# Kernel tuning notes

Measured on AMD Instinct MI355X. Metric: run time of the kernel, lower is better.

## Reference

```python
import jax, jax.numpy as jnp
import numpy as np

N = 100000      # num nodes
F_IN = 512      # dataset.num_features
HID = 32        # hardcoded hidden dim in CRD
C = 40          # dataset.num_classes
E = 3200000     # num edges


def setup_inputs() -> dict:
    key = jax.random.key(0)
    ks = jax.random.split(key, 16)
    def glorot(k, shape):
        lim = float(np.sqrt(6.0 / (shape[0] + shape[1])))
        return jax.random.uniform(k, shape, jnp.float32, -lim, lim)
    inp = {
        "x": jax.random.normal(ks[0], (N, F_IN), dtype=jnp.float32),
        "edge_index": jax.random.randint(ks[1], (2, E), 0, N, dtype=jnp.int32),
        # CRD 1: two GCNConv(F_IN -> HID)
        "W1a": glorot(ks[2], (F_IN, HID)), "b1a": jnp.zeros((HID,), jnp.float32),
        "W1b": glorot(ks[3], (F_IN, HID)), "b1b": jnp.zeros((HID,), jnp.float32),
        # CRD 2: two GCNConv(F_IN -> HID)
        "W2a": glorot(ks[4], (F_IN, HID)), "b2a": jnp.zeros((HID,), jnp.float32),
        "W2b": glorot(ks[5], (F_IN, HID)), "b2b": jnp.zeros((HID,), jnp.float32),
        # CLS: two GCNConv(HID -> C)
        "W3a": glorot(ks[6], (HID, C)), "b3a": jnp.zeros((C,), jnp.float32),
        "W3b": glorot(ks[7], (HID, C)), "b3b": jnp.zeros((C,), jnp.float32),
    }
    return inp


def reference(x, edge_index, W1a, b1a, W1b, b1b, W2a, b2a, W2b, b2b, W3a, b3a, W3b, b3b):
    n = x.shape[0]
    # GCN normalization with self-loops (PyG gcn_norm, cached=True -> shared)
    loop = jnp.arange(n, dtype=edge_index.dtype)
    src = jnp.concatenate([edge_index[0], loop])  # [E+N]
    dst = jnp.concatenate([edge_index[1], loop])
    deg = jax.ops.segment_sum(jnp.ones_like(dst, jnp.float32), dst, num_segments=n)
    dinv = jnp.where(deg > 0, jax.lax.rsqrt(jnp.maximum(deg, 1e-12)), 0.0)
    norm = dinv[src] * dinv[dst]  # [E+N]

    def gcn(h, W, b):
        hw = h @ W                                     # [n, d_out] project first
        msg = hw[src] * norm[:, None]                  # gather + scale
        return jax.ops.segment_sum(msg, dst, num_segments=n) + b  # scatter-add

    # CRD 1 (dropout is identity in eval)
    x1 = jax.nn.relu(gcn(x, W1a, b1a)) + jax.nn.relu(gcn(x, W1b, b1b))
    # CRD 2
    x2 = jax.nn.relu(gcn(x, W2a, b2a)) + jax.nn.relu(gcn(x, W2b, b2b))
    # CLS
    xs = x1 + x2
    out = jax.nn.log_softmax(gcn(xs, W3a, b3a) + gcn(xs, W3b, b3b), axis=1)
    return out
```

## Files before the change

### kernel.cpp

```cpp
#include <hip/hip_runtime.h>
#include <hip/hip_bf16.h>
#include <math.h>

typedef __attribute__((ext_vector_type(8))) short short8;
typedef __attribute__((ext_vector_type(4))) float f32x4;

__device__ inline ushort f2bf(float f) {
    uint u = __builtin_bit_cast(uint, f);
    u += 0x7fffu + ((u >> 16) & 1u);
    return (ushort)(u >> 16);
}
__device__ inline float bf2f(ushort h) {
    return __builtin_bit_cast(float, (uint)h << 16);
}


#define NB   256
#define BKE  2048
#define CAP  16384
#define MAXBE 16384

__device__ inline int bucket_of(int d, int W, float recipW) {
    int g = (int)((float)d * recipW);
    if (g > NB - 1) g = NB - 1;
    while (d < g * W) --g;
    while (d >= (g + 1) * W) ++g;
    return g;
}

__global__ void initcur_kernel(int* __restrict__ cursor256) {
    cursor256[threadIdx.x] = threadIdx.x * CAP;
}

__global__ __launch_bounds__(256) void bucket_kernel(const int* __restrict__ src, const int* __restrict__ dst,
                                                     int* __restrict__ cursor256, int* __restrict__ epk,
                                                     int E, int W, float recipW) {
    __shared__ int hist[NB];
    __shared__ int base[NB];
    int tid = threadIdx.x;
    int e0 = blockIdx.x * BKE;
    int e1 = e0 + BKE; if (e1 > E) e1 = E;
    if (e0 >= E) return;
    hist[tid] = 0;
    __syncthreads();
    int myp[8], myg[8], myr[8];
    #pragma unroll
    for (int it = 0; it < 8; ++it) {
        int e = e0 + tid + it * 256;
        myg[it] = -1;
        if (e < e1) {
            int d = dst[e];
            int g = bucket_of(d, W, recipW);
            myp[it] = src[e] | ((d - g * W) << 17);
            myg[it] = g;
            myr[it] = atomicAdd(&hist[g], 1);
        }
    }
    __syncthreads();
    base[tid] = atomicAdd(&cursor256[tid], hist[tid]);
    __syncthreads();
    #pragma unroll
    for (int it = 0; it < 8; ++it)
        if (myg[it] >= 0)
            epk[base[myg[it]] + myr[it]] = myp[it];
}

__global__ void scanpost_kernel(const int* __restrict__ cursor256, int* __restrict__ bbase) {
    __shared__ int tot[NB];
    int b = threadIdx.x;
    int cnt = cursor256[b] - b * CAP;
    tot[b] = cnt;
    __syncthreads();
    for (int off = 1; off < NB; off <<= 1) {
        int t = (b >= off) ? tot[b - off] : 0;
        __syncthreads();
        tot[b] += t;
        __syncthreads();
    }
    bbase[b] = tot[b] - cnt;
    if (b == NB - 1) bbase[NB] = tot[NB - 1];
}

__global__ __launch_bounds__(256) void sortcsr_kernel(const int* __restrict__ epk,
                                                      const int* __restrict__ bbase,
                                                      int* __restrict__ csr, int* __restrict__ offs,
                                                      float* __restrict__ dinv, int N, int W, int E) {
    __shared__ int lcnt[512];
    __shared__ int lofs[513];
    __shared__ int tmp[256];
    __shared__ int lcsr[MAXBE];
    int b = blockIdx.x;
    int lo = b * W;
    int nloc = N - lo; if (nloc > W) nloc = W; if (nloc < 0) nloc = 0;
    int gbase = bbase[b];
    int cnt = bbase[b + 1] - gbase;
    int ebk = b * CAP;
    int tid = threadIdx.x;
    lcnt[2 * tid] = 0; lcnt[2 * tid + 1] = 0;
    __syncthreads();
    for (int e = tid; e < cnt; e += 256)
        atomicAdd(&lcnt[epk[ebk + e] >> 17], 1);
    __syncthreads();
    int a0 = lcnt[2 * tid], a1 = lcnt[2 * tid + 1];
    int psum = a0 + a1;
    tmp[tid] = psum;
    __syncthreads();
    for (int off = 1; off < 256; off <<= 1) {
        int t = (tid >= off) ? tmp[tid - off] : 0;
        __syncthreads();
        tmp[tid] += t;
        __syncthreads();
    }
    int excl = tmp[tid] - psum;
    lofs[2 * tid] = excl;
    lofs[2 * tid + 1] = excl + a0;
    lcnt[2 * tid] = excl;
    lcnt[2 * tid + 1] = excl + a0;
    if (tid == 255) lofs[512] = tmp[255];
    __syncthreads();
    for (int t = tid; t < nloc; t += 256) {
        offs[lo + t] = gbase + lofs[t];
        int deg = lofs[t + 1] - lofs[t];
        dinv[lo + t] = rsqrtf((float)(deg + 1));
    }
    if (b == NB - 1 && tid == 0) offs[N] = E;
    for (int e = tid; e < cnt; e += 256) {
        int p = epk[ebk + e];
        int pos = atomicAdd(&lcnt[p >> 17], 1);
        int sv = p & 0x1FFFF;
        if (pos < MAXBE) lcsr[pos] = sv;
        else csr[gbase + pos] = sv;
    }
    __syncthreads();
    int ne = cnt; if (ne > MAXBE) ne = MAXBE;
    for (int e = tid; e < ne; e += 256) csr[gbase + e] = lcsr[e];
}


__global__ __launch_bounds__(256) void prep_kernel(const float* __restrict__ W1a, const float* __restrict__ W1b,
                                                   const float* __restrict__ W2a, const float* __restrict__ W2b,
                                                   const float* __restrict__ b1a, const float* __restrict__ b1b,
                                                   const float* __restrict__ b2a, const float* __restrict__ b2b,
                                                   const float* __restrict__ W3a, const float* __restrict__ W3b,
                                                   const float* __restrict__ b3a, const float* __restrict__ b3b,
                                                   ushort* __restrict__ Wt, float* __restrict__ bcat,
                                                   float* __restrict__ W3s, float* __restrict__ b3s) {
    int idx = blockIdx.x * 256 + threadIdx.x;
    if (idx < 128 * 512) {
        int row = idx >> 9, kk = idx & 511;
        int cstore = (kk >> 3) & 7;
        int clog = cstore ^ (row & 7);
        int klog = (kk & ~63) | (clog << 3) | (kk & 7);
        const float* Wsrc = (row < 32) ? W1a : (row < 64) ? W1b : (row < 96) ? W2a : W2b;
        Wt[idx] = f2bf(Wsrc[klog * 32 + (row & 31)]);
    }
    if (idx < 1280) W3s[idx] = W3a[idx] + W3b[idx];
    if (idx < 128) {
        const float* b = (idx < 32) ? b1a : (idx < 64) ? b1b : (idx < 96) ? b2a : b2b;
        bcat[idx] = b[idx & 31];
    }
    if (idx < 40) b3s[idx] = b3a[idx] + b3b[idx];
}


#define GBM 64

__global__ __launch_bounds__(256) void gemm_mfma(const float* __restrict__ X,
                                                 const ushort* __restrict__ Wt,
                                                 const float* __restrict__ dinv,
                                                 ushort* __restrict__ HWp, int N) {
    __shared__ float  Af[64 * 64];
    __shared__ ushort Bl[128 * 64];
    const int tid = threadIdx.x;
    const int lane = tid & 63;
    const int wave = tid >> 6;
    const int rQ = lane & 15, g = lane >> 4;
    const int rowBase = blockIdx.x * GBM;

    const float* agsrc[4];
    #pragma unroll
    for (int i = 0; i < 4; ++i) {
        int q = (i * 4 + wave) * 64 + lane;
        int row = q >> 4, c = q & 15;
        int rowg = rowBase + row; if (rowg > N - 1) rowg = N - 1;
        agsrc[i] = X + (size_t)rowg * 512 + ((c ^ (row & 15)) << 2);
    }
    const ushort* bgsrc[4];
    #pragma unroll
    for (int i = 0; i < 4; ++i) {
        int q = (i * 4 + wave) * 64 + lane;
        int row = q >> 3, c = q & 7;
        bgsrc[i] = Wt + (size_t)row * 512 + (c << 3);
    }

    f32x4 acc[4][2] = {};

#define STAGE(s)                                                              \
    {                                                                         \
        _Pragma("unroll")                                                     \
        for (int i = 0; i < 4; ++i)                                           \
            __builtin_amdgcn_global_load_lds(                                 \
                (const uint*)(agsrc[i] + (s) * 64),                           \
                (uint*)&Af[(i * 4 + wave) * 256], 16, 0, 0);                  \
        _Pragma("unroll")                                                     \
        for (int i = 0; i < 4; ++i)                                           \
            __builtin_amdgcn_global_load_lds(                                 \
                (const uint*)(bgsrc[i] + (s) * 64),                           \
                (uint*)&Bl[(i * 4 + wave) * 512], 16, 0, 0);                  \
    }

#define COMPUTE()                                                             \
    {                                                                         \
        short8 bfr[2][2];                                                     \
        _Pragma("unroll")                                                     \
        for (int ct2 = 0; ct2 < 2; ++ct2) {                                   \
            int brow = wave * 32 + ct2 * 16 + rQ;                             \
            _Pragma("unroll")                                                 \
            for (int sub = 0; sub < 2; ++sub)                                 \
                bfr[ct2][sub] = *(const short8*)(&Bl[brow * 64 + (((sub * 4 + g) ^ (brow & 7)) << 3)]); \
        }                                                                     \
        _Pragma("unroll")                                                     \
        for (int rt = 0; rt < 4; ++rt) {                                      \
            int arw = rt * 16 + rQ;                                           \
            _Pragma("unroll")                                                 \
            for (int sub = 0; sub < 2; ++sub) {                               \
                int c0 = (sub * 4 + g) * 2;                                   \
                float4 lo = *(const float4*)(&Af[arw * 64 + ((c0 ^ (arw & 15)) << 2)]);       \
                float4 hi = *(const float4*)(&Af[arw * 64 + (((c0 + 1) ^ (arw & 15)) << 2)]); \
                union { short8 s8; __hip_bfloat162 h[4]; } u;                 \
                u.h[0] = __float22bfloat162_rn({lo.x, lo.y});                 \
                u.h[1] = __float22bfloat162_rn({lo.z, lo.w});                 \
                u.h[2] = __float22bfloat162_rn({hi.x, hi.y});                 \
                u.h[3] = __float22bfloat162_rn({hi.z, hi.w});                 \
                _Pragma("unroll")                                             \
                for (int ct2 = 0; ct2 < 2; ++ct2)                             \
                    acc[rt][ct2] = __builtin_amdgcn_mfma_f32_16x16x32_bf16(   \
                        u.s8, bfr[ct2][sub], acc[rt][ct2], 0, 0, 0);          \
            }                                                                 \
        }                                                                     \
    }

    for (int s = 0; s < 8; ++s) {
        STAGE(s);
        __syncthreads();
        COMPUTE();
        __syncthreads();
    }

    #pragma unroll
    for (int rt = 0; rt < 4; ++rt) {
        #pragma unroll
        for (int j = 0; j < 4; ++j) {
            int r = rowBase + rt * 16 + g * 4 + j;
            if (r < N) {
                float dv = dinv[r];
                #pragma unroll
                for (int ct2 = 0; ct2 < 2; ++ct2) {
                    int c = wave * 32 + ct2 * 16 + rQ;
                    HWp[(size_t)r * 128 + c] = f2bf(acc[rt][ct2][j] * dv);
                }
            }
        }
    }
#undef STAGE
#undef COMPUTE
}


__global__ __launch_bounds__(256) void agg128(const ushort* __restrict__ HWp, const float* __restrict__ dinv,
                                              const int* __restrict__ offs, const int* __restrict__ csr,
                                              const float* __restrict__ bcat, ushort* __restrict__ xsp, int N) {
    int t = blockIdx.x * 256 + threadIdx.x;
    int node = t >> 4, c = t & 15;
    if (node >= N) return;
    const short8* H = (const short8*)HWp;
    short8 h = H[(size_t)node * 16 + c];
    float a[8];
    #pragma unroll
    for (int i = 0; i < 8; ++i) a[i] = bf2f((ushort)h[i]);
    int j = offs[node];
    int e1 = offs[node + 1];
    int jend = j + ((e1 - j) & ~7);
    for (; j < jend; j += 8) {
        int s[8];
        #pragma unroll
        for (int q = 0; q < 8; ++q) s[q] = csr[j + q];
        short8 v[8];
        #pragma unroll
        for (int q = 0; q < 8; ++q) v[q] = H[(size_t)s[q] * 16 + c];
        #pragma unroll
        for (int q = 0; q < 8; ++q)
            #pragma unroll
            for (int i = 0; i < 8; ++i) a[i] += bf2f((ushort)v[q][i]);
    }
    for (; j < e1; ++j) {
        short8 v = H[(size_t)csr[j] * 16 + c];
        #pragma unroll
        for (int i = 0; i < 8; ++i) a[i] += bf2f((ushort)v[i]);
    }
    float di = dinv[node];
    float4 b0 = *(const float4*)(bcat + c * 8);
    float4 b1 = *(const float4*)(bcat + c * 8 + 4);
    float bb[8] = {b0.x, b0.y, b0.z, b0.w, b1.x, b1.y, b1.z, b1.w};
    float r[8];
    #pragma unroll
    for (int i = 0; i < 8; ++i) r[i] = fmaxf(di * a[i] + bb[i], 0.f);
    #pragma unroll
    for (int i = 0; i < 8; ++i) { r[i] += __shfl_xor(r[i], 4); r[i] += __shfl_xor(r[i], 8); }
    if ((c & 12) == 0) {
        union { short8 s8; ushort us[8]; } o;
        #pragma unroll
        for (int i = 0; i < 8; ++i) o.us[i] = f2bf(r[i] * di);
        *(short8*)(xsp + (size_t)node * 32 + c * 8) = o.s8;
    }
}


__global__ __launch_bounds__(256) void agg32(const ushort* __restrict__ xsp, const float* __restrict__ dinv,
                                             const int* __restrict__ offs, const int* __restrict__ csr,
                                             float* __restrict__ axs, int N) {
    int t = blockIdx.x * 256 + threadIdx.x;
    int node = t >> 2, l = t & 3;
    if (node >= N) return;
    const short8* Xr = (const short8*)xsp;
    short8 h = Xr[(size_t)node * 4 + l];
    float a[8];
    #pragma unroll
    for (int i = 0; i < 8; ++i) a[i] = bf2f((ushort)h[i]);
    int j = offs[node];
    int e1 = offs[node + 1];
    int jend = j + ((e1 - j) & ~7);
    for (; j < jend; j += 8) {
        int s[8];
        #pragma unroll
        for (int q = 0; q < 8; ++q) s[q] = csr[j + q];
        short8 v[8];
        #pragma unroll
        for (int q = 0; q < 8; ++q) v[q] = Xr[(size_t)s[q] * 4 + l];
        #pragma unroll
        for (int q = 0; q < 8; ++q)
            #pragma unroll
            for (int i = 0; i < 8; ++i) a[i] += bf2f((ushort)v[q][i]);
    }
    for (; j < e1; ++j) {
        short8 v = Xr[(size_t)csr[j] * 4 + l];
        #pragma unroll
        for (int i = 0; i < 8; ++i) a[i] += bf2f((ushort)v[i]);
    }
    float di = dinv[node];
    float4 o0 = make_float4(a[0] * di, a[1] * di, a[2] * di, a[3] * di);
    float4 o1 = make_float4(a[4] * di, a[5] * di, a[6] * di, a[7] * di);
    float* dst = axs + (size_t)node * 32 + l * 8;
    *(float4*)dst = o0;
    *(float4*)(dst + 4) = o1;
}


__global__ __launch_bounds__(256) void final_kernel(const float* __restrict__ axs, const float* __restrict__ W3s,
                                                    const float* __restrict__ b3s, float* __restrict__ out, int N) {
    __shared__ float w[32 * 40];
    __shared__ float b[40];
    int tid = threadIdx.x;
    for (int i = tid; i < 1280; i += 256) w[i] = W3s[i];
    if (tid < 40) b[tid] = b3s[tid];
    __syncthreads();
    int i = blockIdx.x * 256 + tid;
    if (i >= N) return;
    float a[32];
    #pragma unroll
    for (int q = 0; q < 8; ++q) {
        float4 v = *(const float4*)(axs + (size_t)i * 32 + q * 4);
        a[q * 4] = v.x; a[q * 4 + 1] = v.y; a[q * 4 + 2] = v.z; a[q * 4 + 3] = v.w;
    }
    float acc[40];
    #pragma unroll
    for (int c = 0; c < 40; ++c) acc[c] = b[c];
    #pragma unroll
    for (int k = 0; k < 32; ++k) {
        float av = a[k];
        #pragma unroll
        for (int c = 0; c < 40; ++c) acc[c] += av * w[k * 40 + c];
    }
    float m = acc[0];
    #pragma unroll
    for (int c = 1; c < 40; ++c) m = fmaxf(m, acc[c]);
    float sum = 0.f;
    #pragma unroll
    for (int c = 0; c < 40; ++c) sum += expf(acc[c] - m);
    float lg = m + logf(sum);
    #pragma unroll
    for (int c = 0; c < 40; ++c) out[(size_t)i * 40 + c] = acc[c] - lg;
}


extern "C" void kernel_launch(void* const* d_in, const int* in_sizes, int n_in,
                              void* d_out, int out_size, void* d_ws, size_t ws_size,
                              hipStream_t stream) {
    const float* x   = (const float*)d_in[0];
    const int*   ei  = (const int*)d_in[1];
    const float* W1a = (const float*)d_in[2];  const float* b1a = (const float*)d_in[3];
    const float* W1b = (const float*)d_in[4];  const float* b1b = (const float*)d_in[5];
    const float* W2a = (const float*)d_in[6];  const float* b2a = (const float*)d_in[7];
    const float* W2b = (const float*)d_in[8];  const float* b2b = (const float*)d_in[9];
    const float* W3a = (const float*)d_in[10]; const float* b3a = (const float*)d_in[11];
    const float* W3b = (const float*)d_in[12]; const float* b3b = (const float*)d_in[13];

    int N = in_sizes[0] / 512;
    int E = in_sizes[1] / 2;
    const int* srcv = ei;
    const int* dstv = ei + E;
    int W = (N + NB - 1) / NB;
    float recipW = 1.0f / (float)W;

    char* ws = (char*)d_ws;
    size_t off = 0;
    auto alloc = [&](size_t bytes) { void* p = ws + off; off = (off + bytes + 255) & ~(size_t)255; return p; };
    int*    offs     = (int*)   alloc((size_t)(N + 1) * 4);
    float*  dinv     = (float*) alloc((size_t)N * 4);
    int*    bbase    = (int*)   alloc((NB + 1) * 4);
    int*    cursor256= (int*)   alloc(NB * 4);
    int*    csr      = (int*)   alloc((size_t)E * 4);
    ushort* Wt       = (ushort*)alloc(128 * 512 * 2);
    float*  bcat     = (float*) alloc(128 * 4);
    float*  W3s      = (float*) alloc(1280 * 4);
    float*  b3s      = (float*) alloc(40 * 4);
    ushort* HWp      = (ushort*)alloc((size_t)N * 128 * 2);
    ushort* xsp      = (ushort*)alloc((size_t)N * 32 * 2);
    float*  axs      = (float*) alloc((size_t)N * 32 * 4);

    int* epk = (int*)HWp;

    initcur_kernel<<<1, 256, 0, stream>>>(cursor256);
    bucket_kernel<<<(E + BKE - 1) / BKE, 256, 0, stream>>>(srcv, dstv, cursor256, epk, E, W, recipW);
    scanpost_kernel<<<1, 256, 0, stream>>>(cursor256, bbase);
    sortcsr_kernel<<<NB, 256, 0, stream>>>(epk, bbase, csr, offs, dinv, N, W, E);
    prep_kernel<<<256, 256, 0, stream>>>(W1a, W1b, W2a, W2b, b1a, b1b, b2a, b2b,
                                         W3a, W3b, b3a, b3b, Wt, bcat, W3s, b3s);
    gemm_mfma<<<(N + GBM - 1) / GBM, 256, 0, stream>>>(x, Wt, dinv, HWp, N);
    agg128<<<((size_t)N * 16 + 255) / 256, 256, 0, stream>>>(HWp, dinv, offs, csr, bcat, xsp, N);
    agg32<<<((size_t)N * 4 + 255) / 256, 256, 0, stream>>>(xsp, dinv, offs, csr, axs, N);
    final_kernel<<<(N + 255) / 256, 256, 0, stream>>>(axs, W3s, b3s, (float*)d_out, N);
}
```

Before: 305.3 us.

## Double-buffer GEMM LDS loads and fuse final projection into agg32

The GEMM kernel now double-buffers its A/B shared tiles. It issues the next stage's global-to-LDS loads before computing the current one, using explicit vmcnt waits and raw s_barriers to hide load latency. The last aggregation kernel is also fused with the 32x40 projection and log-softmax. Each of the 4 lanes per node computes partial logits from its 8 features, combines them with shuffles and writes 10 outputs. This drops the fp32 axs intermediate round trip and one launch, at the cost of doubled LDS use in the GEMM and extra shuffles and register pressure in the fused kernel.

```diff
diff --git a/kernel.cpp b/kernel.cpp
--- a/kernel.cpp
+++ b/kernel.cpp
@@ -169,8 +169,8 @@
                                                  const ushort* __restrict__ Wt,
                                                  const float* __restrict__ dinv,
                                                  ushort* __restrict__ HWp, int N) {
-    __shared__ float  Af[64 * 64];
-    __shared__ ushort Bl[128 * 64];
+    __shared__ float  Af[2][64 * 64];
+    __shared__ ushort Bl[2][128 * 64];
     const int tid = threadIdx.x;
     const int lane = tid & 63;
     const int wave = tid >> 6;
@@ -195,21 +195,21 @@
 
     f32x4 acc[4][2] = {};
 
-#define STAGE(s)                                                              \
+#define STAGE(s, buf)                                                         \
     {                                                                         \
         _Pragma("unroll")                                                     \
         for (int i = 0; i < 4; ++i)                                           \
             __builtin_amdgcn_global_load_lds(                                 \
                 (const uint*)(agsrc[i] + (s) * 64),                           \
-                (uint*)&Af[(i * 4 + wave) * 256], 16, 0, 0);                  \
+                (uint*)&Af[buf][(i * 4 + wave) * 256], 16, 0, 0);             \
         _Pragma("unroll")                                                     \
         for (int i = 0; i < 4; ++i)                                           \
             __builtin_amdgcn_global_load_lds(                                 \
                 (const uint*)(bgsrc[i] + (s) * 64),                           \
-                (uint*)&Bl[(i * 4 + wave) * 512], 16, 0, 0);                  \
-    }
-
-#define COMPUTE()                                                             \
+                (uint*)&Bl[buf][(i * 4 + wave) * 512], 16, 0, 0);             \
+    }
+
+#define COMPUTE(buf)                                                          \
     {                                                                         \
         short8 bfr[2][2];                                                     \
         _Pragma("unroll")                                                     \
@@ -217,7 +217,7 @@
             int brow = wave * 32 + ct2 * 16 + rQ;                             \
             _Pragma("unroll")                                                 \
             for (int sub = 0; sub < 2; ++sub)                                 \
-                bfr[ct2][sub] = *(const short8*)(&Bl[brow * 64 + (((sub * 4 + g) ^ (brow & 7)) << 3)]); \
+                bfr[ct2][sub] = *(const short8*)(&Bl[buf][brow * 64 + (((sub * 4 + g) ^ (brow & 7)) << 3)]); \
         }                                                                     \
         _Pragma("unroll")                                                     \
         for (int rt = 0; rt < 4; ++rt) {                                      \
@@ -225,8 +225,8 @@
             _Pragma("unroll")                                                 \
             for (int sub = 0; sub < 2; ++sub) {                               \
                 int c0 = (sub * 4 + g) * 2;                                   \
-                float4 lo = *(const float4*)(&Af[arw * 64 + ((c0 ^ (arw & 15)) << 2)]);       \
-                float4 hi = *(const float4*)(&Af[arw * 64 + (((c0 + 1) ^ (arw & 15)) << 2)]); \
+                float4 lo = *(const float4*)(&Af[buf][arw * 64 + ((c0 ^ (arw & 15)) << 2)]);       \
+                float4 hi = *(const float4*)(&Af[buf][arw * 64 + (((c0 + 1) ^ (arw & 15)) << 2)]); \
                 union { short8 s8; __hip_bfloat162 h[4]; } u;                 \
                 u.h[0] = __float22bfloat162_rn({lo.x, lo.y});                 \
                 u.h[1] = __float22bfloat162_rn({lo.z, lo.w});                 \
@@ -240,11 +240,19 @@
         }                                                                     \
     }
 
+    STAGE(0, 0);
     for (int s = 0; s < 8; ++s) {
-        STAGE(s);
-        __syncthreads();
-        COMPUTE();
-        __syncthreads();
+        int buf = s & 1;
+        if (s + 1 < 8) {
+            STAGE(s + 1, buf ^ 1);
+            asm volatile("s_waitcnt vmcnt(8)" ::: "memory");
+        } else {
+            asm volatile("s_waitcnt vmcnt(0)" ::: "memory");
+        }
+        __builtin_amdgcn_sched_barrier(0);
+        __builtin_amdgcn_s_barrier();
+        COMPUTE(buf);
+        __builtin_amdgcn_s_barrier();
     }
 
     #pragma unroll
@@ -316,10 +324,18 @@
 }
 
 
-__global__ __launch_bounds__(256) void agg32(const ushort* __restrict__ xsp, const float* __restrict__ dinv,
-                                             const int* __restrict__ offs, const int* __restrict__ csr,
-                                             float* __restrict__ axs, int N) {
-    int t = blockIdx.x * 256 + threadIdx.x;
+__global__ __launch_bounds__(256) void agg32f(const ushort* __restrict__ xsp, const float* __restrict__ dinv,
+                                              const int* __restrict__ offs, const int* __restrict__ csr,
+                                              const float* __restrict__ W3s, const float* __restrict__ b3s,
+                                              float* __restrict__ out, int N) {
+    __shared__ float w[32 * 40];
+    __shared__ float bsh[40];
+    int tid = threadIdx.x;
+    for (int i = tid; i < 1280; i += 256) w[i] = W3s[i];
+    if (tid < 40) bsh[tid] = b3s[tid];
+    __syncthreads();
+
+    int t = blockIdx.x * 256 + tid;
     int node = t >> 2, l = t & 3;
     if (node >= N) return;
     const short8* Xr = (const short8*)xsp;
@@ -348,48 +364,33 @@
         for (int i = 0; i < 8; ++i) a[i] += bf2f((ushort)v[i]);
     }
     float di = dinv[node];
-    float4 o0 = make_float4(a[0] * di, a[1] * di, a[2] * di, a[3] * di);
-    float4 o1 = make_float4(a[4] * di, a[5] * di, a[6] * di, a[7] * di);
-    float* dst = axs + (size_t)node * 32 + l * 8;
-    *(float4*)dst = o0;
-    *(float4*)(dst + 4) = o1;
-}
-
-
-__global__ __launch_bounds__(256) void final_kernel(const float* __restrict__ axs, const float* __restrict__ W3s,
-                                                    const float* __restrict__ b3s, float* __restrict__ out, int N) {
-    __shared__ float w[32 * 40];
-    __shared__ float b[40];
-    int tid = threadIdx.x;
-    for (int i = tid; i < 1280; i += 256) w[i] = W3s[i];
-    if (tid < 40) b[tid] = b3s[tid];
-    __syncthreads();
-    int i = blockIdx.x * 256 + tid;
-    if (i >= N) return;
-    float a[32];
-    #pragma unroll
-    for (int q = 0; q < 8; ++q) {
-        float4 v = *(const float4*)(axs + (size_t)i * 32 + q * 4);
-        a[q * 4] = v.x; a[q * 4 + 1] = v.y; a[q * 4 + 2] = v.z; a[q * 4 + 3] = v.w;
-    }
-    float acc[40];
-    #pragma unroll
-    for (int c = 0; c < 40; ++c) acc[c] = b[c];
-    #pragma unroll
-    for (int k = 0; k < 32; ++k) {
-        float av = a[k];
-        #pragma unroll
-        for (int c = 0; c < 40; ++c) acc[c] += av * w[k * 40 + c];
-    }
-    float m = acc[0];
-    #pragma unroll
-    for (int c = 1; c < 40; ++c) m = fmaxf(m, acc[c]);
+
+    float lg[40];
+    #pragma unroll
+    for (int c = 0; c < 40; ++c) lg[c] = 0.f;
+    #pragma unroll
+    for (int k = 0; k < 8; ++k) {
+        float av = a[k] * di;
+        const float* wr = &w[(l * 8 + k) * 40];
+        #pragma unroll
+        for (int c = 0; c < 40; ++c) lg[c] += av * wr[c];
+    }
+    #pragma unroll
+    for (int c = 0; c < 40; ++c) {
+        lg[c] += __shfl_xor(lg[c], 1);
+        lg[c] += __shfl_xor(lg[c], 2);
+        lg[c] += bsh[c];
+    }
+    float m = lg[0];
+    #pragma unroll
+    for (int c = 1; c < 40; ++c) m = fmaxf(m, lg[c]);
     float sum = 0.f;
     #pragma unroll
-    for (int c = 0; c < 40; ++c) sum += expf(acc[c] - m);
-    float lg = m + logf(sum);
-    #pragma unroll
-    for (int c = 0; c < 40; ++c) out[(size_t)i * 40 + c] = acc[c] - lg;
+    for (int c = 0; c < 40; ++c) sum += expf(lg[c] - m);
+    float lgs = m + logf(sum);
+    float* op = out + (size_t)node * 40 + l * 10;
+    #pragma unroll
+    for (int c = 0; c < 10; ++c) op[c] = lg[l * 10 + c] - lgs;
 }
 
 
@@ -426,7 +427,6 @@
     float*  b3s      = (float*) alloc(40 * 4);
     ushort* HWp      = (ushort*)alloc((size_t)N * 128 * 2);
     ushort* xsp      = (ushort*)alloc((size_t)N * 32 * 2);
-    float*  axs      = (float*) alloc((size_t)N * 32 * 4);
 
     int* epk = (int*)HWp;
 
@@ -438,6 +438,6 @@
                                          W3a, W3b, b3a, b3b, Wt, bcat, W3s, b3s);
     gemm_mfma<<<(N + GBM - 1) / GBM, 256, 0, stream>>>(x, Wt, dinv, HWp, N);
     agg128<<<((size_t)N * 16 + 255) / 256, 256, 0, stream>>>(HWp, dinv, offs, csr, bcat, xsp, N);
-    agg32<<<((size_t)N * 4 + 255) / 256, 256, 0, stream>>>(xsp, dinv, offs, csr, axs, N);
-    final_kernel<<<(N + 255) / 256, 256, 0, stream>>>(axs, W3s, b3s, (float*)d_out, N);
-}
+    agg32f<<<((size_t)N * 4 + 255) / 256, 256, 0, stream>>>(xsp, dinv, offs, csr, W3s, b3s,
+                                                            (float*)d_out, N);
+}
```

Measured after the change: 328.0 us. 7.5% more time.
